# Performance work log

Hardware: AMD Instinct MI355X
Metric: run time of the kernel (lower is better)

The kernel has to match this reference:

```python
import jax, jax.numpy as jnp
import numpy as np

BN_EPS = 1e-5


def setup_inputs() -> dict:
    key = jax.random.key(0)
    ks = jax.random.split(key, 10)
    d = {}
    # EEG-style input: [B, 1, T, electrodes]
    d["x"] = jax.random.normal(ks[0], (512, 1, 1125, 5), dtype=jnp.float32)
    # conv_time: Conv2d(1, 40, (25, 1)) with bias
    d["conv_time_w"] = jax.random.normal(ks[1], (40, 1, 25, 1), dtype=jnp.float32) * 0.05
    d["conv_time_b"] = jax.random.normal(ks[2], (40,), dtype=jnp.float32) * 0.05
    # conv_spat: Conv2d(40, 40, (1, 5), bias=False)
    d["conv_spat_w"] = jax.random.normal(ks[3], (40, 40, 1, 5), dtype=jnp.float32) * 0.05
    # BatchNorm2d(40), eval mode (running stats)
    d["bn_gamma"] = jnp.ones((40,), jnp.float32)
    d["bn_beta"] = jnp.zeros((40,), jnp.float32)
    d["bn_mean"] = jnp.zeros((40,), jnp.float32)
    d["bn_var"] = jnp.ones((40,), jnp.float32)
    # LSTM(input=40, hidden=10): torch layout W_ih [4H, in], W_hh [4H, H]
    d["w_ih"] = jax.random.normal(ks[4], (40, 40), dtype=jnp.float32) * 0.1
    d["w_hh"] = jax.random.normal(ks[5], (40, 10), dtype=jnp.float32) * 0.1
    d["b_ih"] = jax.random.normal(ks[6], (40,), dtype=jnp.float32) * 0.1
    d["b_hh"] = jax.random.normal(ks[7], (40,), dtype=jnp.float32) * 0.1
    # classifier: Linear(10, 2)
    d["fc_w"] = jax.random.normal(ks[8], (2, 10), dtype=jnp.float32) * 0.1
    d["fc_b"] = jnp.zeros((2,), jnp.float32)
    return d


def reference(x, conv_time_w, conv_time_b, conv_spat_w,
              bn_gamma, bn_beta, bn_mean, bn_var,
              w_ih, w_hh, b_ih, b_hh, fc_w, fc_b):
    dn = ("NCHW", "OIHW", "NCHW")
    # conv over time: [B,1,T,5] -> [B,40,T-24,5]
    h = jax.lax.conv_general_dilated(x, conv_time_w, (1, 1), "VALID", dimension_numbers=dn)
    h = h + conv_time_b[None, :, None, None]
    # conv over electrodes: [B,40,T-24,5] -> [B,40,T-24,1]
    h = jax.lax.conv_general_dilated(h, conv_spat_w, (1, 1), "VALID", dimension_numbers=dn)
    # BatchNorm2d (eval, running stats)
    scale = bn_gamma / jnp.sqrt(bn_var + BN_EPS)
    h = h * scale[None, :, None, None] + (bn_beta - bn_mean * scale)[None, :, None, None]
    # AvgPool2d kernel (25,1) stride (5,1): -> [B,40,L,1], L = (T-24-25)//5 + 1
    h = jax.lax.reduce_window(h, 0.0, jax.lax.add, (1, 1, 25, 1), (1, 1, 5, 1), "VALID") / 25.0
    # Dropout2d in eval mode = identity
    # squeeze width + transpose(1,2): [B,40,L] -> [B,L,40]
    h = jnp.transpose(h[..., 0], (0, 2, 1))
    B = h.shape[0]
    H = w_hh.shape[1]  # hidden = 10
    # precompute input-to-gate projection for all timesteps: [L, B, 4H]
    xg = jnp.einsum("blf,gf->lbg", h, w_ih) + b_ih + b_hh

    def step(carry, xt):
        h_prev, c_prev = carry
        gates = xt + h_prev @ w_hh.T          # [B, 4H]
        i, f, g, o = jnp.split(gates, 4, axis=-1)
        i = jax.nn.sigmoid(i)
        f = jax.nn.sigmoid(f)
        g = jnp.tanh(g)
        o = jax.nn.sigmoid(o)
        c = f * c_prev + i * g
        hn = o * jnp.tanh(c)
        return (hn, c), None

    init = (jnp.zeros((B, H), h.dtype), jnp.zeros((B, H), h.dtype))
    (h_last, _), _ = jax.lax.scan(step, init, xg)  # return_seq=False -> last hidden
    return h_last @ fc_w.T + fc_b  # [B, 2]
```

## Files before the change

### kernel.cpp

```cpp
#include <hip/hip_runtime.h>

#define LOG2E 1.44269504088896340736f

typedef float v2f __attribute__((ext_vector_type(2)));

__device__ __forceinline__ float bf2f(unsigned short u) {
    union { unsigned u32; float f; } v; v.u32 = ((unsigned)u) << 16; return v.f;
}
__device__ __forceinline__ unsigned short f2bf(float f) {
    union { float f; unsigned u32; } v; v.f = f;
    unsigned r = (v.u32 + 0x7FFFu + ((v.u32 >> 16) & 1u)) >> 16;
    return (unsigned short)r;
}
__device__ __forceinline__ bool probe_bf16(const void* gma) {
    return *(const unsigned int*)gma == 0x3F803F80u;
}
__device__ __forceinline__ float ldmix(const void* p, int i, bool bf) {
    return bf ? bf2f(((const unsigned short*)p)[i]) : ((const float*)p)[i];
}
__device__ __forceinline__ float dpp_shl(float x, const int n) {
    int r;
    if (n == 1)      r = __builtin_amdgcn_update_dpp(0, __float_as_int(x), 0x101, 0xF, 0xF, true);
    else if (n == 2) r = __builtin_amdgcn_update_dpp(0, __float_as_int(x), 0x102, 0xF, 0xF, true);
    else             r = __builtin_amdgcn_update_dpp(0, __float_as_int(x), 0x103, 0xF, 0xF, true);
    return __int_as_float(r);
}
__device__ __forceinline__ float rdlane(float v, int l) {
    return __int_as_float(__builtin_amdgcn_readlane(__float_as_int(v), l));
}
#if __has_builtin(__builtin_amdgcn_exp2f)
__device__ __forceinline__ float fexp2(float x) { return __builtin_amdgcn_exp2f(x); }
#else
__device__ __forceinline__ float fexp2(float x) {
    float r; asm("v_exp_f32 %0, %1" : "=v"(r) : "v"(x)); return r;
}
#endif

__global__ __launch_bounds__(1024) void prep_kernel(
    const void* __restrict__ ctw,
    const void* __restrict__ ctb,
    const void* __restrict__ csw,
    const void* __restrict__ gma,
    const void* __restrict__ bta,
    const void* __restrict__ mea,
    const void* __restrict__ var,
    const void* __restrict__ wih,
    const void* __restrict__ bih,
    const void* __restrict__ bhh,
    float* __restrict__ Wg,
    float* __restrict__ Bg)
{
    __shared__ float s_wt[1000];
    __shared__ float s_bt[40];
    __shared__ float s_sp[8000];
    __shared__ float s_wih[1600];
    __shared__ float s_scale[40], s_shift[40];
    __shared__ float s_Wc[5000];
    __shared__ float s_P[5200];
    __shared__ float s_Bc[40];
    __shared__ float s_Wp[9920];

    const int t = threadIdx.x;
    const bool bf = probe_bf16(gma);

    for (int i = t; i < 1000; i += 1024) s_wt[i] = ldmix(ctw, i, bf);
    for (int i = t; i < 8000; i += 1024) s_sp[i] = ldmix(csw, i, bf);
    for (int i = t; i < 1600; i += 1024) s_wih[i] = ldmix(wih, i, bf);
    if (t < 40) {
        s_bt[t] = ldmix(ctb, t, bf);
        float sc = ldmix(gma, t, bf) * rsqrtf(ldmix(var, t, bf) + 1e-5f);
        s_scale[t] = sc;
        s_shift[t] = ldmix(bta, t, bf) - ldmix(mea, t, bf) * sc;
    }
    __syncthreads();

    if (t < 200) {
        const int oc = t / 5, kq = (t % 5) * 5;
        float acc[5][5];
        #pragma unroll
        for (int q = 0; q < 5; ++q)
            #pragma unroll
            for (int e = 0; e < 5; ++e) acc[q][e] = 0.f;
        for (int ic = 0; ic < 40; ++ic) {
            float wtv[5], spv[5];
            #pragma unroll
            for (int q = 0; q < 5; ++q) wtv[q] = s_wt[ic * 25 + kq + q];
            #pragma unroll
            for (int e = 0; e < 5; ++e) spv[e] = s_sp[(oc * 40 + ic) * 5 + e];
            #pragma unroll
            for (int q = 0; q < 5; ++q)
                #pragma unroll
                for (int e = 0; e < 5; ++e) acc[q][e] = fmaf(wtv[q], spv[e], acc[q][e]);
        }
        const float sc = s_scale[oc];
        #pragma unroll
        for (int q = 0; q < 5; ++q)
            #pragma unroll
            for (int e = 0; e < 5; ++e)
                s_Wc[(oc * 25 + kq + q) * 5 + e] = acc[q][e] * sc;
    }
    if (t >= 512 && t < 552) {
        const int oc = t - 512;
        float a = 0.f;
        for (int ic = 0; ic < 40; ++ic) {
            float se = 0.f;
            #pragma unroll
            for (int e = 0; e < 5; ++e) se += s_sp[(oc * 40 + ic) * 5 + e];
            a = fmaf(se, s_bt[ic], a);
        }
        s_Bc[oc] = a * s_scale[oc] + s_shift[oc];
    }
    __syncthreads();

    if (t < 200) {
        const int oc = t / 5, e = t % 5;
        float run = 0.f;
        s_P[oc * 130 + e] = 0.f;
        for (int k = 0; k < 25; ++k) {
            run += s_Wc[(oc * 25 + k) * 5 + e];
            s_P[oc * 130 + (k + 1) * 5 + e] = run;
        }
    }
    __syncthreads();

    for (int i = t; i < 9800; i += 1024) {
        const int oc = i / 245, rem = i % 245, j = rem / 5, e = rem % 5;
        const int lo = j - 24 > 0 ? j - 24 : 0;
        const int hi = j < 24 ? j : 24;
        float val = (s_P[oc * 130 + (hi + 1) * 5 + e] - s_P[oc * 130 + lo * 5 + e]) * 0.04f;
        s_Wp[oc * 248 + rem] = val;
    }
    if (t < 120) s_Wp[(t / 3) * 248 + 245 + (t % 3)] = 0.f;
    __syncthreads();

    if (t < 620) {
        const int gp = t / 31, ko = t % 31;
        const int g0 = 2 * gp, kf0 = 8 * ko;
        float acc0[8], acc1[8];
        #pragma unroll
        for (int q = 0; q < 8; ++q) { acc0[q] = 0.f; acc1[q] = 0.f; }
        for (int oc = 0; oc < 40; ++oc) {
            const float4 pa = *reinterpret_cast<const float4*>(&s_Wp[oc * 248 + kf0]);
            const float4 pb = *reinterpret_cast<const float4*>(&s_Wp[oc * 248 + kf0 + 4]);
            const float wa = s_wih[g0 * 40 + oc];
            const float wb = s_wih[(g0 + 1) * 40 + oc];
            acc0[0] = fmaf(wa, pa.x, acc0[0]); acc0[1] = fmaf(wa, pa.y, acc0[1]);
            acc0[2] = fmaf(wa, pa.z, acc0[2]); acc0[3] = fmaf(wa, pa.w, acc0[3]);
            acc0[4] = fmaf(wa, pb.x, acc0[4]); acc0[5] = fmaf(wa, pb.y, acc0[5]);
            acc0[6] = fmaf(wa, pb.z, acc0[6]); acc0[7] = fmaf(wa, pb.w, acc0[7]);
            acc1[0] = fmaf(wb, pa.x, acc1[0]); acc1[1] = fmaf(wb, pa.y, acc1[1]);
            acc1[2] = fmaf(wb, pa.z, acc1[2]); acc1[3] = fmaf(wb, pa.w, acc1[3]);
            acc1[4] = fmaf(wb, pb.x, acc1[4]); acc1[5] = fmaf(wb, pb.y, acc1[5]);
            acc1[6] = fmaf(wb, pb.z, acc1[6]); acc1[7] = fmaf(wb, pb.w, acc1[7]);
        }
        #pragma unroll
        for (int q = 0; q < 8; ++q) {
            const int kf = kf0 + q;
            const int base = (kf >> 2) * 160 + (kf & 3);
            Wg[base + g0 * 4]       = acc0[q];
            Wg[base + (g0 + 1) * 4] = acc1[q];
        }
    }
    if (t >= 640 && t < 680) {
        const int g = t - 640;
        float a = ldmix(bih, g, bf) + ldmix(bhh, g, bf);
        for (int oc = 0; oc < 40; ++oc) a = fmaf(s_wih[g * 40 + oc], s_Bc[oc], a);
        Bg[g] = a;
    }
}

__global__ __launch_bounds__(256, 2) void fused_kernel(
    const void* __restrict__ x,
    const float* __restrict__ Wg,
    const float* __restrict__ Bg,
    const void* __restrict__ whh_p,
    const void* __restrict__ fcw_p,
    const void* __restrict__ fcb_p,
    const void* __restrict__ gma,
    void* __restrict__ out)
{
    __shared__ float u[9216];

    const int b   = blockIdx.x;
    const int tid = threadIdx.x;
    const bool bf = probe_bf16(gma);

    if (bf) {
        const unsigned short* xp = (const unsigned short*)x + b * 5625;
        for (int i = tid; i < 5625; i += 256) u[i] = bf2f(xp[i]);
    } else {
        const float* xp = (const float*)x + b * 5625;
        for (int i = tid; i < 5625; i += 256) u[i] = xp[i];
    }
    for (int i = 5625 + tid; i < 6144; i += 256) u[i] = 0.f;
    for (int i = 8856 + tid; i < 9216; i += 256) u[i] = 0.f;
    __syncthreads();

    const int wave  = __builtin_amdgcn_readfirstlane(tid >> 6);
    const int lane  = tid & 63;
    const int gb    = 20 * (wave & 1);
    const int lbase = 108 * (wave >> 1);
    const int l0 = lbase + lane;
    const int l1 = l0 + 64;
    const int a0 = 25 * l0, a1 = 25 * l1;

    v2f acc[20];
    #pragma unroll
    for (int gi = 0; gi < 20; ++gi) {
        float bgv = Bg[gb + gi];
        acc[gi] = (v2f){bgv, bgv};
    }

    int dz = 0;
    asm volatile("" : "+v"(dz));
    const float4* wq = reinterpret_cast<const float4*>(Wg) + gb + dz;

    for (int k4 = 0; k4 < 62; ++k4) {
        const int k = 4 * k4;
        v2f xv0 = (v2f){ u[a0 + k],     u[a1 + k]     };
        v2f xv1 = (v2f){ u[a0 + k + 1], u[a1 + k + 1] };
        v2f xv2 = (v2f){ u[a0 + k + 2], u[a1 + k + 2] };
        v2f xv3 = (v2f){ u[a0 + k + 3], u[a1 + k + 3] };
        #pragma unroll
        for (int gi = 0; gi < 20; ++gi) {
            const float4 w = wq[gi];
            acc[gi] += xv0 * w.x;
            acc[gi] += xv1 * w.y;
            acc[gi] += xv2 * w.z;
            acc[gi] += xv3 * w.w;
        }
        wq += 40;
    }
    __syncthreads();

    #pragma unroll
    for (int gi = 0; gi < 20; ++gi) {
        u[l0 * 41 + gb + gi] = acc[gi].x;
        if (lane < 44) u[l1 * 41 + gb + gi] = acc[gi].y;
    }
    __syncthreads();

    if (wave != 0) return;

    const int j   = lane >> 2;
    const int jt  = lane & 3;
    const int jj  = j < 10 ? j : 9;
    const int gl  = 10 * jt + jj;

    const float L2   = 2.0f * LOG2E;
    const float kmul = (jt == 2) ?  L2 : -LOG2E;
    const float aact = (jt == 2) ? -2.0f : (jt == 0 ? L2 : 1.0f);
    const float bact = (jt == 2) ?  1.0f : 0.0f;

    float whhr[10];
    #pragma unroll
    for (int m = 0; m < 10; ++m) whhr[m] = kmul * ldmix(whh_p, gl * 10 + m, bf);

    float xb[6];
    #pragma unroll
    for (int p = 0; p < 6; ++p) xb[p] = kmul * u[p * 41 + gl];

    float cs = 0.f, h = 0.f;

    for (int l = 0; l < 216; l += 6) {
        #pragma unroll
        for (int s = 0; s < 6; ++s) {
            float xv = xb[s];
            xb[s] = kmul * u[(l + s + 6) * 41 + gl];
            float h0 = rdlane(h, 0),  h1 = rdlane(h, 4),  h2 = rdlane(h, 8);
            float h3 = rdlane(h, 12), h4 = rdlane(h, 16), h5 = rdlane(h, 20);
            float h6 = rdlane(h, 24), h7 = rdlane(h, 28), h8 = rdlane(h, 32);
            float h9 = rdlane(h, 36);
            float p0 = fmaf(whhr[0], h0, xv);
            float p1 = whhr[1] * h1;
            float p2 = whhr[2] * h2;
            float p3 = whhr[3] * h3;
            p0 = fmaf(whhr[4], h4, p0);
            p1 = fmaf(whhr[5], h5, p1);
            p2 = fmaf(whhr[6], h6, p2);
            p3 = fmaf(whhr[7], h7, p3);
            p0 = fmaf(whhr[8], h8, p0);
            p1 = fmaf(whhr[9], h9, p1);
            float accg = (p0 + p2) + (p1 + p3);
            float tt  = fexp2(accg);
            float rr  = __builtin_amdgcn_rcpf(1.0f + tt);
            float act = fmaf(aact, rr, bact);
            float fv = dpp_shl(act, 1);
            float gv = dpp_shl(act, 2);
            float ov = dpp_shl(act, 3);
            cs = fmaf(fv, cs, act * gv);
            float t2 = fexp2(cs);
            float r2 = __builtin_amdgcn_rcpf(1.0f + t2);
            float th = fmaf(-2.0f, r2, 1.0f);
            h = ov * th;
        }
    }

    float w0[10], w1[10];
    #pragma unroll
    for (int m = 0; m < 10; ++m) {
        w0[m] = ldmix(fcw_p, m, bf);
        w1[m] = ldmix(fcw_p, 10 + m, bf);
    }
    float o0 = ldmix(fcb_p, 0, bf), o1 = ldmix(fcb_p, 1, bf);
    #pragma unroll
    for (int m = 0; m < 10; ++m) {
        float hm = rdlane(h, 4 * m);
        o0 = fmaf(w0[m], hm, o0);
        o1 = fmaf(w1[m], hm, o1);
    }
    if (lane == 0) {
        if (bf) {
            ((unsigned short*)out)[b * 2]     = f2bf(o0);
            ((unsigned short*)out)[b * 2 + 1] = f2bf(o1);
        } else {
            ((float*)out)[b * 2]     = o0;
            ((float*)out)[b * 2 + 1] = o1;
        }
    }
}

extern "C" void kernel_launch(void* const* d_in, const int* in_sizes, int n_in,
                              void* d_out, int out_size, void* d_ws, size_t ws_size,
                              hipStream_t stream) {
    const void* x    = d_in[0];
    const void* ctw  = d_in[1];
    const void* ctb  = d_in[2];
    const void* csw  = d_in[3];
    const void* gma  = d_in[4];
    const void* bta  = d_in[5];
    const void* mea  = d_in[6];
    const void* var  = d_in[7];
    const void* wih  = d_in[8];
    const void* whh  = d_in[9];
    const void* bih  = d_in[10];
    const void* bhh  = d_in[11];
    const void* fcw  = d_in[12];
    const void* fcb  = d_in[13];

    char* ws = (char*)d_ws;
    float* Wg = (float*)ws;
    float* Bg = (float*)(ws + 40 * 248 * 4);

    prep_kernel<<<1, 1024, 0, stream>>>(ctw, ctb, csw, gma, bta, mea, var,
                                        wih, bih, bhh, Wg, Bg);
    fused_kernel<<<512, 256, 0, stream>>>(x, Wg, Bg, whh, fcw, fcb, gma, d_out);
}
```

Baseline: 196.6 us.

## Stage fused-conv weights in VGPRs per lane and broadcast via readlane

The prep kernel now writes the fused gate weights in a new lane-chunked layout, zero-padded to 256 taps, and Bg moves to a new offset to make room. The main kernel no longer reads weights with per-iteration global/scalar float4 loads. Instead each lane loads a chunk of 64 taps into registers, prefetched one chunk ahead, and the inner loop broadcasts each weight with readlane. This is meant to remove the repeated weight-load latency from the inner FMA loop. In exchange it adds readlane instructions and register pressure, and it processes 256 taps where 248 were processed before.

```diff
diff --git a/kernel.cpp b/kernel.cpp
--- a/kernel.cpp
+++ b/kernel.cpp
@@ -63,6 +63,7 @@
     const int t = threadIdx.x;
     const bool bf = probe_bf16(gma);
 
+    for (int i = t; i < 10240; i += 1024) Wg[i] = 0.f;
     for (int i = t; i < 1000; i += 1024) s_wt[i] = ldmix(ctw, i, bf);
     for (int i = t; i < 8000; i += 1024) s_sp[i] = ldmix(csw, i, bf);
     for (int i = t; i < 1600; i += 1024) s_wih[i] = ldmix(wih, i, bf);
@@ -153,12 +154,13 @@
             acc1[4] = fmaf(wb, pb.x, acc1[4]); acc1[5] = fmaf(wb, pb.y, acc1[5]);
             acc1[6] = fmaf(wb, pb.z, acc1[6]); acc1[7] = fmaf(wb, pb.w, acc1[7]);
         }
+        const int hh = g0 / 20, gia = g0 % 20;
         #pragma unroll
         for (int q = 0; q < 8; ++q) {
-            const int kf = kf0 + q;
-            const int base = (kf >> 2) * 160 + (kf & 3);
-            Wg[base + g0 * 4]       = acc0[q];
-            Wg[base + (g0 + 1) * 4] = acc1[q];
+            const int kf = kf0 + q, k4 = kf >> 2, kc = kf & 3;
+            const int base = ((hh * 4 + (k4 >> 4)) * 320 + (k4 & 15)) * 4 + kc;
+            Wg[base + (gia * 16) * 4]       = acc0[q];
+            Wg[base + ((gia + 1) * 16) * 4] = acc1[q];
         }
     }
     if (t >= 640 && t < 680) {
@@ -198,7 +200,8 @@
 
     const int wave  = __builtin_amdgcn_readfirstlane(tid >> 6);
     const int lane  = tid & 63;
-    const int gb    = 20 * (wave & 1);
+    const int half  = wave & 1;
+    const int gb    = 20 * half;
     const int lbase = 108 * (wave >> 1);
     const int l0 = lbase + lane;
     const int l1 = l0 + 64;
@@ -211,26 +214,45 @@
         acc[gi] = (v2f){bgv, bgv};
     }
 
-    int dz = 0;
-    asm volatile("" : "+v"(dz));
-    const float4* wq = reinterpret_cast<const float4*>(Wg) + gb + dz;
-
-    for (int k4 = 0; k4 < 62; ++k4) {
-        const int k = 4 * k4;
-        v2f xv0 = (v2f){ u[a0 + k],     u[a1 + k]     };
-        v2f xv1 = (v2f){ u[a0 + k + 1], u[a1 + k + 1] };
-        v2f xv2 = (v2f){ u[a0 + k + 2], u[a1 + k + 2] };
-        v2f xv3 = (v2f){ u[a0 + k + 3], u[a1 + k + 3] };
-        #pragma unroll
-        for (int gi = 0; gi < 20; ++gi) {
-            const float4 w = wq[gi];
-            acc[gi] += xv0 * w.x;
-            acc[gi] += xv1 * w.y;
-            acc[gi] += xv2 * w.z;
-            acc[gi] += xv3 * w.w;
-        }
-        wq += 40;
-    }
+    const float4* wq = reinterpret_cast<const float4*>(Wg) + half * 1280 + lane;
+
+    float4 wA[5], wB[5];
+    #pragma unroll
+    for (int i = 0; i < 5; ++i) wA[i] = wq[i * 64];
+    wq += 320;
+
+    for (int c = 0; c < 4; ++c) {
+        if (c < 3) {
+            #pragma unroll
+            for (int i = 0; i < 5; ++i) wB[i] = wq[i * 64];
+            wq += 320;
+        }
+        const int kb = c << 6;
+        #pragma unroll
+        for (int s = 0; s < 16; ++s) {
+            const int k = kb + (s << 2);
+            v2f xv0 = (v2f){ u[a0 + k],     u[a1 + k]     };
+            v2f xv1 = (v2f){ u[a0 + k + 1], u[a1 + k + 1] };
+            v2f xv2 = (v2f){ u[a0 + k + 2], u[a1 + k + 2] };
+            v2f xv3 = (v2f){ u[a0 + k + 3], u[a1 + k + 3] };
+            #pragma unroll
+            for (int gi = 0; gi < 20; ++gi) {
+                const int bb = gi >> 2;
+                const int ln = ((gi & 3) << 4) + s;
+                const float wx = rdlane(wA[bb].x, ln);
+                const float wy = rdlane(wA[bb].y, ln);
+                const float wz = rdlane(wA[bb].z, ln);
+                const float ww = rdlane(wA[bb].w, ln);
+                acc[gi] += xv0 * wx;
+                acc[gi] += xv1 * wy;
+                acc[gi] += xv2 * wz;
+                acc[gi] += xv3 * ww;
+            }
+        }
+        #pragma unroll
+        for (int i = 0; i < 5; ++i) wA[i] = wB[i];
+    }
+
     __syncthreads();
 
     #pragma unroll
@@ -340,7 +362,7 @@
 
     char* ws = (char*)d_ws;
     float* Wg = (float*)ws;
-    float* Bg = (float*)(ws + 40 * 248 * 4);
+    float* Bg = (float*)(ws + 40960);
 
     prep_kernel<<<1, 1024, 0, stream>>>(ctw, ctb, csw, gma, bta, mea, var,
                                         wih, bih, bhh, Wg, Bg);
```

Measured after the change: 172.3 us. 12.4% less time.
